# Optimization experiments

Hardware: AMD Instinct MI355X
Metric: run time of the kernel (lower is better)

## Reference

```python
import jax, jax.numpy as jnp
import numpy as np

EMB_DIM = 64
B, S, D = 64, 1024, 64

def setup_inputs() -> dict:
    key = jax.random.key(0)
    k1, k2, k3, k4, k5 = jax.random.split(key, 5)
    return {
        "query": jax.random.normal(k1, (B, S, D), dtype=jnp.float32),
        "key": jax.random.normal(k2, (B, S, D), dtype=jnp.float32),
        "value": jax.random.normal(k3, (B, S, D), dtype=jnp.float32),
        "a_key": jax.random.normal(k4, (S, S, D), dtype=jnp.float32),
        "a_value": jax.random.normal(k5, (S, S, D), dtype=jnp.float32),
    }

def reference(query, key, value, a_key, a_value):
    scale = jnp.sqrt(jnp.asarray(EMB_DIM, dtype=query.dtype))
    # standard content-content scores: [B, Sq, Sk]
    qk = jnp.einsum("bqd,bkd->bqk", query, key)
    # relative key scores: a_key is [Sq, Sk, D]; contract over D per query position
    rel_qk = jnp.einsum("bqd,qkd->bqk", query, a_key)
    attn = jax.nn.softmax((qk + rel_qk) / scale, axis=-1)
    # content values + relative values
    qkv = jnp.einsum("bqk,bkd->bqd", attn, value)
    rel_qkv = jnp.einsum("bqk,qkd->bqd", attn, a_value)
    return qkv + rel_qkv, attn
```

## Files before the change

### kernel.cpp

```cpp
#include <hip/hip_runtime.h>
#include <stdint.h>

#define S_ 1024
#define D_ 64
#define B_ 64

typedef short short8 __attribute__((ext_vector_type(8)));
typedef unsigned short ushort8 __attribute__((ext_vector_type(8)));
typedef float f32x4 __attribute__((ext_vector_type(4)));

__device__ __forceinline__ unsigned short f2bf(float x) {
    uint32_t u = __builtin_bit_cast(uint32_t, x);
    return (unsigned short)((u + 0x7FFFu + ((u >> 16) & 1u)) >> 16);
}
__device__ __forceinline__ float bf2f(unsigned short b) {
    return __builtin_bit_cast(float, ((uint32_t)b) << 16);
}
__device__ __forceinline__ uint32_t pack2(float a, float b) {
    return (uint32_t)f2bf(a) | ((uint32_t)f2bf(b) << 16);
}
__device__ __forceinline__ int scidx(int row, int k) {
    return (((row << 10) + (k & ~7)) ^ ((row & 15) << 3)) + (k & 7);
}

__global__ __launch_bounds__(256) void k1_qk(const float* __restrict__ Q,
                                             const float* __restrict__ Kk,
                                             float* __restrict__ qk) {
    __shared__ __align__(16) unsigned short Qs[128][72];
    __shared__ __align__(16) unsigned short Ks[128][72];
    const int bx = blockIdx.x;
    const int b  = bx >> 6;
    const int q0 = ((bx >> 3) & 7) << 7;
    const int k0 = (bx & 7) << 7;
    const int t  = threadIdx.x;
#pragma unroll
    for (int i = 0; i < 8; ++i) {
        int f = (i << 8) + t;
        int row = f >> 4, c = (f & 15) << 2;
        float4 v = *reinterpret_cast<const float4*>(&Q[((size_t)(b * S_ + q0 + row) << 6) + c]);
        *reinterpret_cast<uint2*>(&Qs[row][c]) = make_uint2(pack2(v.x, v.y), pack2(v.z, v.w));
        float4 u = *reinterpret_cast<const float4*>(&Kk[((size_t)(b * S_ + k0 + row) << 6) + c]);
        *reinterpret_cast<uint2*>(&Ks[row][c]) = make_uint2(pack2(u.x, u.y), pack2(u.z, u.w));
    }
    __syncthreads();
    const int l = t & 63, w = t >> 6, lr = l & 15, lg = l >> 4;
    short8 a[2][2];
#pragma unroll
    for (int mi = 0; mi < 2; ++mi)
#pragma unroll
        for (int h = 0; h < 2; ++h)
            a[mi][h] = *reinterpret_cast<const short8*>(&Qs[((w * 2 + mi) << 4) + lr][h * 32 + lg * 8]);
    f32x4 acc[2][8] = {};
#pragma unroll
    for (int n = 0; n < 8; ++n) {
        short8 b0 = *reinterpret_cast<const short8*>(&Ks[(n << 4) + lr][lg * 8]);
        short8 b1 = *reinterpret_cast<const short8*>(&Ks[(n << 4) + lr][32 + lg * 8]);
#pragma unroll
        for (int mi = 0; mi < 2; ++mi) {
            acc[mi][n] = __builtin_amdgcn_mfma_f32_16x16x32_bf16(a[mi][0], b0, acc[mi][n], 0, 0, 0);
            acc[mi][n] = __builtin_amdgcn_mfma_f32_16x16x32_bf16(a[mi][1], b1, acc[mi][n], 0, 0, 0);
        }
    }
#pragma unroll
    for (int mi = 0; mi < 2; ++mi)
#pragma unroll
        for (int n = 0; n < 8; ++n)
#pragma unroll
            for (int r = 0; r < 4; ++r) {
                int qq = q0 + ((w * 2 + mi) << 4) + (lg << 2) + r;
                int kc = k0 + (n << 4) + lr;
                qk[((size_t)(b * S_ + qq) << 10) + kc] = acc[mi][n][r];
            }
}

__device__ __forceinline__ void tpose_store(unsigned short (*Tls)[72], float4 p,
                                            int i, int t) {
    const int l = t & 63, w = t >> 6, lr = l & 15, lg = l >> 4;
    float v0 = p.x, v1 = p.y, v2 = p.z, v3 = p.w;
    float y0 = __shfl_xor(v0, 16), y1 = __shfl_xor(v1, 16),
          y2 = __shfl_xor(v2, 16), y3 = __shfl_xor(v3, 16);
    bool o = (lg & 1);
    float n0 = o ? y1 : v0, n1 = o ? v1 : y0, n2 = o ? y3 : v2, n3 = o ? v3 : y2;
    float z0 = __shfl_xor(n0, 32), z1 = __shfl_xor(n1, 32),
          z2 = __shfl_xor(n2, 32), z3 = __shfl_xor(n3, 32);
    bool h = (lg & 2);
    float T0 = h ? z2 : n0, T1 = h ? z3 : n1, T2 = h ? n2 : z0, T3 = h ? n3 : z1;
    int d = (lr << 2) + lg, kb = (i << 4) + (w << 2);
    *reinterpret_cast<uint2*>(&Tls[d][kb]) = make_uint2(pack2(T0, T1), pack2(T2, T3));
}

__global__ __launch_bounds__(256) void k2_mid(const float* __restrict__ Q,
                                              const float* __restrict__ AK,
                                              const float* __restrict__ AV,
                                              float* __restrict__ attn,
                                              float* __restrict__ outp) {
    __shared__ __align__(16) unsigned short Sc[32 * 1024];
    __shared__ __align__(16) unsigned short Qs[32][72];
    __shared__ __align__(16) unsigned short Ak[64][72];
    __shared__ float invs[32];
    const float SCL = 0.18033688011112042f;
    const int j = blockIdx.x;
    const int xcd = j & 7, slot = j >> 3;
    const int q  = xcd * 128 + (slot >> 1);
    const int b0 = (slot & 1) << 5;
    const int t  = threadIdx.x;
    const int l = t & 63, w = t >> 6, lr = l & 15, lg = l >> 4;

#pragma unroll
    for (int i = 0; i < 2; ++i) {
        int f = (i << 8) + t;
        int row = f >> 4, c = (f & 15) << 2;
        float4 v = *reinterpret_cast<const float4*>(&Q[((size_t)((b0 + row) * S_ + q) << 6) + c]);
        *reinterpret_cast<uint2*>(&Qs[row][c]) =
            make_uint2(pack2(v.x * SCL, v.y * SCL), pack2(v.z * SCL, v.w * SCL));
    }
#pragma unroll
    for (int i = 0; i < 32; ++i) {
        int col = t << 2;
        float4 v = *reinterpret_cast<const float4*>(&attn[((size_t)((b0 + i) * S_ + q) << 10) + col]);
        *reinterpret_cast<uint2*>(&Sc[scidx(i, col)]) =
            make_uint2(pack2(v.x * SCL, v.y * SCL), pack2(v.z * SCL, v.w * SCL));
    }
    const float* akbase = &AK[(size_t)q << 16];
    float4 pf[4];
#pragma unroll
    for (int i = 0; i < 4; ++i) {
        int f = (i << 8) + t;
        pf[i] = *reinterpret_cast<const float4*>(&akbase[((size_t)(f >> 4) << 6) + ((f & 15) << 2)]);
    }
    __syncthreads();

    short8 qa[2][2];
#pragma unroll
    for (int mi = 0; mi < 2; ++mi)
#pragma unroll
        for (int h = 0; h < 2; ++h)
            qa[mi][h] = *reinterpret_cast<const short8*>(&Qs[(mi << 4) + lr][(h << 5) + (lg << 3)]);

    for (int tt = 0; tt < 16; ++tt) {
        __syncthreads();
#pragma unroll
        for (int i = 0; i < 4; ++i) {
            int f = (i << 8) + t;
            int row = f >> 4, c = (f & 15) << 2;
            *reinterpret_cast<uint2*>(&Ak[row][c]) =
                make_uint2(pack2(pf[i].x, pf[i].y), pack2(pf[i].z, pf[i].w));
        }
        __syncthreads();
        if (tt < 15) {
            const float* nb = akbase + (((size_t)(tt + 1)) << 12);
#pragma unroll
            for (int i = 0; i < 4; ++i) {
                int f = (i << 8) + t;
                pf[i] = *reinterpret_cast<const float4*>(&nb[((size_t)(f >> 4) << 6) + ((f & 15) << 2)]);
            }
        }
        short8 bb0 = *reinterpret_cast<const short8*>(&Ak[(w << 4) + lr][lg << 3]);
        short8 bb1 = *reinterpret_cast<const short8*>(&Ak[(w << 4) + lr][32 + (lg << 3)]);
        int kcol = (tt << 6) + (w << 4) + lr;
#pragma unroll
        for (int mi = 0; mi < 2; ++mi) {
            f32x4 c;
#pragma unroll
            for (int r = 0; r < 4; ++r) c[r] = bf2f(Sc[scidx((mi << 4) + (lg << 2) + r, kcol)]);
            c = __builtin_amdgcn_mfma_f32_16x16x32_bf16(qa[mi][0], bb0, c, 0, 0, 0);
            c = __builtin_amdgcn_mfma_f32_16x16x32_bf16(qa[mi][1], bb1, c, 0, 0, 0);
#pragma unroll
            for (int r = 0; r < 4; ++r) Sc[scidx((mi << 4) + (lg << 2) + r, kcol)] = f2bf(c[r]);
        }
    }
    __syncthreads();

    {
        int row = t >> 3, ch = t & 7;
        float m = -1e30f;
#pragma unroll
        for (int i = 0; i < 16; ++i) {
            int k = (((i << 3) + ch) << 3);
            ushort8 v = *reinterpret_cast<const ushort8*>(&Sc[scidx(row, k)]);
#pragma unroll
            for (int jj = 0; jj < 8; ++jj) m = fmaxf(m, bf2f(v[jj]));
        }
#pragma unroll
        for (int d = 1; d < 8; d <<= 1) m = fmaxf(m, __shfl_xor(m, d));
        float s = 0.f;
#pragma unroll
        for (int i = 0; i < 16; ++i) {
            int k = (((i << 3) + ch) << 3);
            int idx = scidx(row, k);
            ushort8 v = *reinterpret_cast<const ushort8*>(&Sc[idx]);
            ushort8 e;
#pragma unroll
            for (int jj = 0; jj < 8; ++jj) {
                float ev = exp2f(bf2f(v[jj]) - m);
                s += ev;
                e[jj] = f2bf(ev);
            }
            *reinterpret_cast<ushort8*>(&Sc[idx]) = e;
        }
#pragma unroll
        for (int d = 1; d < 8; d <<= 1) s += __shfl_xor(s, d);
        float inv = 1.0f / s;
        if (ch == 0) invs[row] = inv;
    }
    __syncthreads();

    const float* avbase = &AV[(size_t)q << 16];
#pragma unroll
    for (int i = 0; i < 4; ++i) {
        int f = (i << 8) + t;
        pf[i] = *reinterpret_cast<const float4*>(&avbase[((size_t)(f >> 4) << 6) + ((f & 15) << 2)]);
    }
#pragma unroll
    for (int i = 0; i < 32; ++i) {
        int col = t << 2;
        uint2 u = *reinterpret_cast<const uint2*>(&Sc[scidx(i, col)]);
        float inv = invs[i];
        float4 o = make_float4(bf2f((unsigned short)(u.x & 0xffff)) * inv,
                               bf2f((unsigned short)(u.x >> 16)) * inv,
                               bf2f((unsigned short)(u.y & 0xffff)) * inv,
                               bf2f((unsigned short)(u.y >> 16)) * inv);
        *reinterpret_cast<float4*>(&attn[((size_t)((b0 + i) * S_ + q) << 10) + col]) = o;
    }

    f32x4 oacc[2] = {};
    for (int tt = 0; tt < 16; ++tt) {
        __syncthreads();
#pragma unroll
        for (int i = 0; i < 4; ++i) tpose_store(Ak, pf[i], i, t);
        __syncthreads();
        if (tt < 15) {
            const float* nb = avbase + (((size_t)(tt + 1)) << 12);
#pragma unroll
            for (int i = 0; i < 4; ++i) {
                int f = (i << 8) + t;
                pf[i] = *reinterpret_cast<const float4*>(&nb[((size_t)(f >> 4) << 6) + ((f & 15) << 2)]);
            }
        }
        short8 bb0 = *reinterpret_cast<const short8*>(&Ak[(w << 4) + lr][lg << 3]);
        short8 bb1 = *reinterpret_cast<const short8*>(&Ak[(w << 4) + lr][32 + (lg << 3)]);
#pragma unroll
        for (int mi = 0; mi < 2; ++mi) {
            short8 ea0 = *reinterpret_cast<const short8*>(&Sc[scidx((mi << 4) + lr, (tt << 6) + (lg << 3))]);
            short8 ea1 = *reinterpret_cast<const short8*>(&Sc[scidx((mi << 4) + lr, (tt << 6) + 32 + (lg << 3))]);
            oacc[mi] = __builtin_amdgcn_mfma_f32_16x16x32_bf16(ea0, bb0, oacc[mi], 0, 0, 0);
            oacc[mi] = __builtin_amdgcn_mfma_f32_16x16x32_bf16(ea1, bb1, oacc[mi], 0, 0, 0);
        }
    }
#pragma unroll
    for (int mi = 0; mi < 2; ++mi)
#pragma unroll
        for (int r = 0; r < 4; ++r) {
            int brow = (mi << 4) + (lg << 2) + r;
            outp[((size_t)((b0 + brow) * S_ + q) << 6) + (w << 4) + lr] = oacc[mi][r] * invs[brow];
        }
}

__global__ __launch_bounds__(256) void k3_pv(const float* __restrict__ V,
                                             const float* __restrict__ attn,
                                             float* __restrict__ outp) {
    __shared__ __align__(16) unsigned short At[64][72];
    __shared__ __align__(16) unsigned short Vt[64][72];
    const int b  = blockIdx.x >> 4;
    const int q0 = (blockIdx.x & 15) << 6;
    const int t  = threadIdx.x;
    const int l = t & 63, w = t >> 6, lr = l & 15, lg = l >> 4;
    float4 pa[4], pv[4];
#pragma unroll
    for (int i = 0; i < 4; ++i) {
        int f = (i << 8) + t;
        int row = f >> 4, c = (f & 15) << 2;
        pa[i] = *reinterpret_cast<const float4*>(&attn[((size_t)(b * S_ + q0 + row) << 10) + c]);
        pv[i] = *reinterpret_cast<const float4*>(&V[((size_t)(b * S_ + row) << 6) + c]);
    }
    f32x4 acc[4] = {};
    for (int tt = 0; tt < 16; ++tt) {
        __syncthreads();
#pragma unroll
        for (int i = 0; i < 4; ++i) {
            int f = (i << 8) + t;
            int row = f >> 4, c = (f & 15) << 2;
            *reinterpret_cast<uint2*>(&At[row][c]) =
                make_uint2(pack2(pa[i].x, pa[i].y), pack2(pa[i].z, pa[i].w));
            tpose_store(Vt, pv[i], i, t);
        }
        __syncthreads();
        if (tt < 15) {
#pragma unroll
            for (int i = 0; i < 4; ++i) {
                int f = (i << 8) + t;
                int row = f >> 4, c = (f & 15) << 2;
                pa[i] = *reinterpret_cast<const float4*>(
                    &attn[((size_t)(b * S_ + q0 + row) << 10) + ((tt + 1) << 6) + c]);
                pv[i] = *reinterpret_cast<const float4*>(
                    &V[((size_t)(b * S_ + ((tt + 1) << 6) + row) << 6) + c]);
            }
        }
        short8 a0 = *reinterpret_cast<const short8*>(&At[(w << 4) + lr][lg * 8]);
        short8 a1 = *reinterpret_cast<const short8*>(&At[(w << 4) + lr][32 + lg * 8]);
#pragma unroll
        for (int n = 0; n < 4; ++n) {
            short8 b0 = *reinterpret_cast<const short8*>(&Vt[(n << 4) + lr][lg * 8]);
            short8 b1 = *reinterpret_cast<const short8*>(&Vt[(n << 4) + lr][32 + lg * 8]);
            acc[n] = __builtin_amdgcn_mfma_f32_16x16x32_bf16(a0, b0, acc[n], 0, 0, 0);
            acc[n] = __builtin_amdgcn_mfma_f32_16x16x32_bf16(a1, b1, acc[n], 0, 0, 0);
        }
    }
#pragma unroll
    for (int n = 0; n < 4; ++n)
#pragma unroll
        for (int r = 0; r < 4; ++r) {
            size_t idx = ((size_t)(b * S_ + q0 + (w << 4) + (lg << 2) + r) << 6) + (n << 4) + lr;
            outp[idx] += acc[n][r];
        }
}

extern "C" void kernel_launch(void* const* d_in, const int* in_sizes, int n_in,
                              void* d_out, int out_size, void* d_ws, size_t ws_size,
                              hipStream_t stream) {
    (void)in_sizes; (void)n_in; (void)out_size; (void)d_ws; (void)ws_size;
    const float* Q  = (const float*)d_in[0];
    const float* K  = (const float*)d_in[1];
    const float* V  = (const float*)d_in[2];
    const float* AK = (const float*)d_in[3];
    const float* AV = (const float*)d_in[4];
    float* outp = (float*)d_out;
    float* attn = outp + (size_t)B_ * S_ * D_;

    k1_qk <<<dim3(64 * 8 * 8), dim3(256), 0, stream>>>(Q, K, attn);
    k2_mid<<<dim3(2048),       dim3(256), 0, stream>>>(Q, AK, AV, attn, outp);
    k3_pv <<<dim3(64 * 16),    dim3(256), 0, stream>>>(V, attn, outp);
}
```

Baseline: 425.7 us.

## Double-buffer relative key/value prefetch and fuse qk add into softmax pass

```diff
diff --git a/kernel.cpp b/kernel.cpp
--- a/kernel.cpp
+++ b/kernel.cpp
@@ -8,6 +8,9 @@
 typedef short short8 __attribute__((ext_vector_type(8)));
 typedef unsigned short ushort8 __attribute__((ext_vector_type(8)));
 typedef float f32x4 __attribute__((ext_vector_type(4)));
+
+#define LBAR() do { asm volatile("s_waitcnt lgkmcnt(0)" ::: "memory"); \
+                    __builtin_amdgcn_s_barrier(); } while (0)
 
 __device__ __forceinline__ unsigned short f2bf(float x) {
     uint32_t u = __builtin_bit_cast(uint32_t, x);
@@ -114,80 +117,105 @@
         *reinterpret_cast<uint2*>(&Qs[row][c]) =
             make_uint2(pack2(v.x * SCL, v.y * SCL), pack2(v.z * SCL, v.w * SCL));
     }
-#pragma unroll
-    for (int i = 0; i < 32; ++i) {
-        int col = t << 2;
-        float4 v = *reinterpret_cast<const float4*>(&attn[((size_t)((b0 + i) * S_ + q) << 10) + col]);
-        *reinterpret_cast<uint2*>(&Sc[scidx(i, col)]) =
-            make_uint2(pack2(v.x * SCL, v.y * SCL), pack2(v.z * SCL, v.w * SCL));
-    }
     const float* akbase = &AK[(size_t)q << 16];
-    float4 pf[4];
-#pragma unroll
-    for (int i = 0; i < 4; ++i) {
-        int f = (i << 8) + t;
-        pf[i] = *reinterpret_cast<const float4*>(&akbase[((size_t)(f >> 4) << 6) + ((f & 15) << 2)]);
-    }
-    __syncthreads();
-
+    float4 pf[2][4];
+#pragma unroll
+    for (int d2 = 0; d2 < 2; ++d2)
+#pragma unroll
+        for (int i = 0; i < 4; ++i) {
+            int f = (i << 8) + t;
+            pf[d2][i] = *reinterpret_cast<const float4*>(
+                &akbase[(size_t)(d2 << 12) + ((size_t)(f >> 4) << 6) + ((f & 15) << 2)]);
+        }
+    LBAR();
     short8 qa[2][2];
 #pragma unroll
-    for (int mi = 0; mi < 2; ++mi)
+    for (int bh = 0; bh < 2; ++bh)
 #pragma unroll
         for (int h = 0; h < 2; ++h)
-            qa[mi][h] = *reinterpret_cast<const short8*>(&Qs[(mi << 4) + lr][(h << 5) + (lg << 3)]);
+            qa[bh][h] = *reinterpret_cast<const short8*>(&Qs[(bh << 4) + lr][(h << 5) + (lg << 3)]);
 
     for (int tt = 0; tt < 16; ++tt) {
-        __syncthreads();
+        LBAR();
 #pragma unroll
         for (int i = 0; i < 4; ++i) {
             int f = (i << 8) + t;
             int row = f >> 4, c = (f & 15) << 2;
             *reinterpret_cast<uint2*>(&Ak[row][c]) =
-                make_uint2(pack2(pf[i].x, pf[i].y), pack2(pf[i].z, pf[i].w));
-        }
-        __syncthreads();
-        if (tt < 15) {
-            const float* nb = akbase + (((size_t)(tt + 1)) << 12);
+                make_uint2(pack2(pf[tt & 1][i].x, pf[tt & 1][i].y),
+                           pack2(pf[tt & 1][i].z, pf[tt & 1][i].w));
+        }
+        LBAR();
+        if (tt < 14) {
+            const float* nb = akbase + (((size_t)(tt + 2)) << 12);
 #pragma unroll
             for (int i = 0; i < 4; ++i) {
                 int f = (i << 8) + t;
-                pf[i] = *reinterpret_cast<const float4*>(&nb[((size_t)(f >> 4) << 6) + ((f & 15) << 2)]);
-            }
-        }
-        short8 bb0 = *reinterpret_cast<const short8*>(&Ak[(w << 4) + lr][lg << 3]);
-        short8 bb1 = *reinterpret_cast<const short8*>(&Ak[(w << 4) + lr][32 + (lg << 3)]);
-        int kcol = (tt << 6) + (w << 4) + lr;
-#pragma unroll
-        for (int mi = 0; mi < 2; ++mi) {
-            f32x4 c;
-#pragma unroll
-            for (int r = 0; r < 4; ++r) c[r] = bf2f(Sc[scidx((mi << 4) + (lg << 2) + r, kcol)]);
-            c = __builtin_amdgcn_mfma_f32_16x16x32_bf16(qa[mi][0], bb0, c, 0, 0, 0);
-            c = __builtin_amdgcn_mfma_f32_16x16x32_bf16(qa[mi][1], bb1, c, 0, 0, 0);
-#pragma unroll
-            for (int r = 0; r < 4; ++r) Sc[scidx((mi << 4) + (lg << 2) + r, kcol)] = f2bf(c[r]);
-        }
-    }
-    __syncthreads();
+                pf[tt & 1][i] = *reinterpret_cast<const float4*>(
+                    &nb[((size_t)(f >> 4) << 6) + ((f & 15) << 2)]);
+            }
+        }
+        short8 ak0 = *reinterpret_cast<const short8*>(&Ak[(w << 4) + lr][lg << 3]);
+        short8 ak1 = *reinterpret_cast<const short8*>(&Ak[(w << 4) + lr][32 + (lg << 3)]);
+        int kbase = (tt << 6) + (w << 4) + (lg << 2);
+#pragma unroll
+        for (int bh = 0; bh < 2; ++bh) {
+            f32x4 c = {};
+            c = __builtin_amdgcn_mfma_f32_16x16x32_bf16(ak0, qa[bh][0], c, 0, 0, 0);
+            c = __builtin_amdgcn_mfma_f32_16x16x32_bf16(ak1, qa[bh][1], c, 0, 0, 0);
+            *reinterpret_cast<uint2*>(&Sc[scidx((bh << 4) + lr, kbase)]) =
+                make_uint2(pack2(c[0], c[1]), pack2(c[2], c[3]));
+        }
+    }
+    LBAR();
+
+    const float* avbase = &AV[(size_t)q << 16];
+    float4 pv[2][4];
+#pragma unroll
+    for (int d2 = 0; d2 < 2; ++d2)
+#pragma unroll
+        for (int i = 0; i < 4; ++i) {
+            int f = (i << 8) + t;
+            pv[d2][i] = *reinterpret_cast<const float4*>(
+                &avbase[(size_t)(d2 << 12) + ((size_t)(f >> 4) << 6) + ((f & 15) << 2)]);
+        }
 
     {
         int row = t >> 3, ch = t & 7;
+        float* qkrow = &attn[((size_t)((b0 + row) * S_ + q) << 10)];
         float m = -1e30f;
-#pragma unroll
+        float4 g0 = *reinterpret_cast<const float4*>(&qkrow[ch << 3]);
+        float4 g1 = *reinterpret_cast<const float4*>(&qkrow[(ch << 3) + 4]);
         for (int i = 0; i < 16; ++i) {
-            int k = (((i << 3) + ch) << 3);
-            ushort8 v = *reinterpret_cast<const ushort8*>(&Sc[scidx(row, k)]);
-#pragma unroll
-            for (int jj = 0; jj < 8; ++jj) m = fmaxf(m, bf2f(v[jj]));
+            float4 c0 = g0, c1 = g1;
+            if (i < 15) {
+                int kn = (((i + 1) << 3) + ch) << 3;
+                g0 = *reinterpret_cast<const float4*>(&qkrow[kn]);
+                g1 = *reinterpret_cast<const float4*>(&qkrow[kn + 4]);
+            }
+            int idx = scidx(row, ((i << 3) + ch) << 3);
+            ushort8 rel = *reinterpret_cast<const ushort8*>(&Sc[idx]);
+            float s0 = fmaf(c0.x, SCL, bf2f(rel[0]));
+            float s1 = fmaf(c0.y, SCL, bf2f(rel[1]));
+            float s2 = fmaf(c0.z, SCL, bf2f(rel[2]));
+            float s3 = fmaf(c0.w, SCL, bf2f(rel[3]));
+            float s4 = fmaf(c1.x, SCL, bf2f(rel[4]));
+            float s5 = fmaf(c1.y, SCL, bf2f(rel[5]));
+            float s6 = fmaf(c1.z, SCL, bf2f(rel[6]));
+            float s7 = fmaf(c1.w, SCL, bf2f(rel[7]));
+            m = fmaxf(m, fmaxf(fmaxf(fmaxf(s0, s1), fmaxf(s2, s3)),
+                               fmaxf(fmaxf(s4, s5), fmaxf(s6, s7))));
+            ushort8 o;
+            o[0] = f2bf(s0); o[1] = f2bf(s1); o[2] = f2bf(s2); o[3] = f2bf(s3);
+            o[4] = f2bf(s4); o[5] = f2bf(s5); o[6] = f2bf(s6); o[7] = f2bf(s7);
+            *reinterpret_cast<ushort8*>(&Sc[idx]) = o;
         }
 #pragma unroll
         for (int d = 1; d < 8; d <<= 1) m = fmaxf(m, __shfl_xor(m, d));
         float s = 0.f;
-#pragma unroll
+#pragma unroll 4
         for (int i = 0; i < 16; ++i) {
-            int k = (((i << 3) + ch) << 3);
-            int idx = scidx(row, k);
+            int idx = scidx(row, ((i << 3) + ch) << 3);
             ushort8 v = *reinterpret_cast<const ushort8*>(&Sc[idx]);
             ushort8 e;
 #pragma unroll
@@ -202,39 +230,32 @@
         for (int d = 1; d < 8; d <<= 1) s += __shfl_xor(s, d);
         float inv = 1.0f / s;
         if (ch == 0) invs[row] = inv;
-    }
-    __syncthreads();
-
-    const float* avbase = &AV[(size_t)q << 16];
-#pragma unroll
-    for (int i = 0; i < 4; ++i) {
-        int f = (i << 8) + t;
-        pf[i] = *reinterpret_cast<const float4*>(&avbase[((size_t)(f >> 4) << 6) + ((f & 15) << 2)]);
-    }
-#pragma unroll
-    for (int i = 0; i < 32; ++i) {
-        int col = t << 2;
-        uint2 u = *reinterpret_cast<const uint2*>(&Sc[scidx(i, col)]);
-        float inv = invs[i];
-        float4 o = make_float4(bf2f((unsigned short)(u.x & 0xffff)) * inv,
-                               bf2f((unsigned short)(u.x >> 16)) * inv,
-                               bf2f((unsigned short)(u.y & 0xffff)) * inv,
-                               bf2f((unsigned short)(u.y >> 16)) * inv);
-        *reinterpret_cast<float4*>(&attn[((size_t)((b0 + i) * S_ + q) << 10) + col]) = o;
+#pragma unroll 4
+        for (int i = 0; i < 16; ++i) {
+            int k = ((i << 3) + ch) << 3;
+            ushort8 v = *reinterpret_cast<const ushort8*>(&Sc[scidx(row, k)]);
+            float4 o0 = make_float4(bf2f(v[0]) * inv, bf2f(v[1]) * inv,
+                                    bf2f(v[2]) * inv, bf2f(v[3]) * inv);
+            float4 o1 = make_float4(bf2f(v[4]) * inv, bf2f(v[5]) * inv,
+                                    bf2f(v[6]) * inv, bf2f(v[7]) * inv);
+            *reinterpret_cast<float4*>(&qkrow[k]) = o0;
+            *reinterpret_cast<float4*>(&qkrow[k + 4]) = o1;
+        }
     }
 
     f32x4 oacc[2] = {};
     for (int tt = 0; tt < 16; ++tt) {
-        __syncthreads();
-#pragma unroll
-        for (int i = 0; i < 4; ++i) tpose_store(Ak, pf[i], i, t);
-        __syncthreads();
-        if (tt < 15) {
-            const float* nb = avbase + (((size_t)(tt + 1)) << 12);
+        LBAR();
+#pragma unroll
+        for (int i = 0; i < 4; ++i) tpose_store(Ak, pv[tt & 1][i], i, t);
+        LBAR();
+        if (tt < 14) {
+            const float* nb = avbase + (((size_t)(tt + 2)) << 12);
 #pragma unroll
             for (int i = 0; i < 4; ++i) {
                 int f = (i << 8) + t;
-                pf[i] = *reinterpret_cast<const float4*>(&nb[((size_t)(f >> 4) << 6) + ((f & 15) << 2)]);
+                pv[tt & 1][i] = *reinterpret_cast<const float4*>(
+                    &nb[((size_t)(f >> 4) << 6) + ((f & 15) << 2)]);
             }
         }
         short8 bb0 = *reinterpret_cast<const short8*>(&Ak[(w << 4) + lr][lg << 3]);
@@ -275,7 +296,7 @@
     }
     f32x4 acc[4] = {};
     for (int tt = 0; tt < 16; ++tt) {
-        __syncthreads();
+        LBAR();
 #pragma unroll
         for (int i = 0; i < 4; ++i) {
             int f = (i << 8) + t;
@@ -284,7 +305,7 @@
                 make_uint2(pack2(pa[i].x, pa[i].y), pack2(pa[i].z, pa[i].w));
             tpose_store(Vt, pv[i], i, t);
         }
-        __syncthreads();
+        LBAR();
         if (tt < 15) {
 #pragma unroll
             for (int i = 0; i < 4; ++i) {
```

Measured after the change: 648.9 us. +52.4%, slower.

## Fuse content scores into exp pass and drop max-subtraction in softmax

Applied to the files above, without the earlier changes.

```diff
diff --git a/kernel.cpp b/kernel.cpp
--- a/kernel.cpp
+++ b/kernel.cpp
@@ -114,13 +114,6 @@
         *reinterpret_cast<uint2*>(&Qs[row][c]) =
             make_uint2(pack2(v.x * SCL, v.y * SCL), pack2(v.z * SCL, v.w * SCL));
     }
-#pragma unroll
-    for (int i = 0; i < 32; ++i) {
-        int col = t << 2;
-        float4 v = *reinterpret_cast<const float4*>(&attn[((size_t)((b0 + i) * S_ + q) << 10) + col]);
-        *reinterpret_cast<uint2*>(&Sc[scidx(i, col)]) =
-            make_uint2(pack2(v.x * SCL, v.y * SCL), pack2(v.z * SCL, v.w * SCL));
-    }
     const float* akbase = &AK[(size_t)q << 16];
     float4 pf[4];
 #pragma unroll
@@ -129,13 +122,12 @@
         pf[i] = *reinterpret_cast<const float4*>(&akbase[((size_t)(f >> 4) << 6) + ((f & 15) << 2)]);
     }
     __syncthreads();
-
     short8 qa[2][2];
 #pragma unroll
-    for (int mi = 0; mi < 2; ++mi)
+    for (int bh = 0; bh < 2; ++bh)
 #pragma unroll
         for (int h = 0; h < 2; ++h)
-            qa[mi][h] = *reinterpret_cast<const short8*>(&Qs[(mi << 4) + lr][(h << 5) + (lg << 3)]);
+            qa[bh][h] = *reinterpret_cast<const short8*>(&Qs[(bh << 4) + lr][(h << 5) + (lg << 3)]);
 
     for (int tt = 0; tt < 16; ++tt) {
         __syncthreads();
@@ -155,63 +147,59 @@
                 pf[i] = *reinterpret_cast<const float4*>(&nb[((size_t)(f >> 4) << 6) + ((f & 15) << 2)]);
             }
         }
-        short8 bb0 = *reinterpret_cast<const short8*>(&Ak[(w << 4) + lr][lg << 3]);
-        short8 bb1 = *reinterpret_cast<const short8*>(&Ak[(w << 4) + lr][32 + (lg << 3)]);
-        int kcol = (tt << 6) + (w << 4) + lr;
-#pragma unroll
-        for (int mi = 0; mi < 2; ++mi) {
-            f32x4 c;
-#pragma unroll
-            for (int r = 0; r < 4; ++r) c[r] = bf2f(Sc[scidx((mi << 4) + (lg << 2) + r, kcol)]);
-            c = __builtin_amdgcn_mfma_f32_16x16x32_bf16(qa[mi][0], bb0, c, 0, 0, 0);
-            c = __builtin_amdgcn_mfma_f32_16x16x32_bf16(qa[mi][1], bb1, c, 0, 0, 0);
-#pragma unroll
-            for (int r = 0; r < 4; ++r) Sc[scidx((mi << 4) + (lg << 2) + r, kcol)] = f2bf(c[r]);
-        }
+        short8 ak0 = *reinterpret_cast<const short8*>(&Ak[(w << 4) + lr][lg << 3]);
+        short8 ak1 = *reinterpret_cast<const short8*>(&Ak[(w << 4) + lr][32 + (lg << 3)]);
+        int kbase = (tt << 6) + (w << 4) + (lg << 2);
+#pragma unroll
+        for (int bh = 0; bh < 2; ++bh) {
+            f32x4 c = {};
+            c = __builtin_amdgcn_mfma_f32_16x16x32_bf16(ak0, qa[bh][0], c, 0, 0, 0);
+            c = __builtin_amdgcn_mfma_f32_16x16x32_bf16(ak1, qa[bh][1], c, 0, 0, 0);
+            *reinterpret_cast<uint2*>(&Sc[scidx((bh << 4) + lr, kbase)]) =
+                make_uint2(pack2(c[0], c[1]), pack2(c[2], c[3]));
+        }
+    }
+    __syncthreads();
+
+    const float* avbase = &AV[(size_t)q << 16];
+    float4 pv[4];
+#pragma unroll
+    for (int i = 0; i < 4; ++i) {
+        int f = (i << 8) + t;
+        pv[i] = *reinterpret_cast<const float4*>(
+            &avbase[((size_t)(f >> 4) << 6) + ((f & 15) << 2)]);
+    }
+
+#pragma unroll 8
+    for (int i = 0; i < 32; ++i) {
+        int col = t << 2;
+        float4 g = *reinterpret_cast<const float4*>(&attn[((size_t)((b0 + i) * S_ + q) << 10) + col]);
+        int idx = scidx(i, col);
+        uint2 cu = *reinterpret_cast<const uint2*>(&Sc[idx]);
+        float p0 = exp2f(fmaf(g.x, SCL, bf2f((unsigned short)(cu.x & 0xffff))));
+        float p1 = exp2f(fmaf(g.y, SCL, bf2f((unsigned short)(cu.x >> 16))));
+        float p2 = exp2f(fmaf(g.z, SCL, bf2f((unsigned short)(cu.y & 0xffff))));
+        float p3 = exp2f(fmaf(g.w, SCL, bf2f((unsigned short)(cu.y >> 16))));
+        *reinterpret_cast<uint2*>(&Sc[idx]) = make_uint2(pack2(p0, p1), pack2(p2, p3));
     }
     __syncthreads();
 
     {
         int row = t >> 3, ch = t & 7;
-        float m = -1e30f;
-#pragma unroll
+        float s = 0.f;
+#pragma unroll 4
         for (int i = 0; i < 16; ++i) {
-            int k = (((i << 3) + ch) << 3);
-            ushort8 v = *reinterpret_cast<const ushort8*>(&Sc[scidx(row, k)]);
-#pragma unroll
-            for (int jj = 0; jj < 8; ++jj) m = fmaxf(m, bf2f(v[jj]));
-        }
-#pragma unroll
-        for (int d = 1; d < 8; d <<= 1) m = fmaxf(m, __shfl_xor(m, d));
-        float s = 0.f;
-#pragma unroll
-        for (int i = 0; i < 16; ++i) {
-            int k = (((i << 3) + ch) << 3);
-            int idx = scidx(row, k);
-            ushort8 v = *reinterpret_cast<const ushort8*>(&Sc[idx]);
-            ushort8 e;
-#pragma unroll
-            for (int jj = 0; jj < 8; ++jj) {
-                float ev = exp2f(bf2f(v[jj]) - m);
-                s += ev;
-                e[jj] = f2bf(ev);
-            }
-            *reinterpret_cast<ushort8*>(&Sc[idx]) = e;
+            ushort8 v = *reinterpret_cast<const ushort8*>(&Sc[scidx(row, (((i << 3) + ch) << 3))]);
+#pragma unroll
+            for (int jj = 0; jj < 8; ++jj) s += bf2f(v[jj]);
         }
 #pragma unroll
         for (int d = 1; d < 8; d <<= 1) s += __shfl_xor(s, d);
-        float inv = 1.0f / s;
-        if (ch == 0) invs[row] = inv;
-    }
-    __syncthreads();
-
-    const float* avbase = &AV[(size_t)q << 16];
-#pragma unroll
-    for (int i = 0; i < 4; ++i) {
-        int f = (i << 8) + t;
-        pf[i] = *reinterpret_cast<const float4*>(&avbase[((size_t)(f >> 4) << 6) + ((f & 15) << 2)]);
-    }
-#pragma unroll
+        if (ch == 0) invs[row] = 1.0f / s;
+    }
+    __syncthreads();
+
+#pragma unroll 8
     for (int i = 0; i < 32; ++i) {
         int col = t << 2;
         uint2 u = *reinterpret_cast<const uint2*>(&Sc[scidx(i, col)]);
@@ -227,14 +215,15 @@
     for (int tt = 0; tt < 16; ++tt) {
         __syncthreads();
 #pragma unroll
-        for (int i = 0; i < 4; ++i) tpose_store(Ak, pf[i], i, t);
+        for (int i = 0; i < 4; ++i) tpose_store(Ak, pv[i], i, t);
         __syncthreads();
         if (tt < 15) {
             const float* nb = avbase + (((size_t)(tt + 1)) << 12);
 #pragma unroll
             for (int i = 0; i < 4; ++i) {
                 int f = (i << 8) + t;
-                pf[i] = *reinterpret_cast<const float4*>(&nb[((size_t)(f >> 4) << 6) + ((f & 15) << 2)]);
+                pv[i] = *reinterpret_cast<const float4*>(
+                    &nb[((size_t)(f >> 4) << 6) + ((f & 15) << 2)]);
             }
         }
         short8 bb0 = *reinterpret_cast<const short8*>(&Ak[(w << 4) + lr][lg << 3]);
```

Measured after the change: 453.5 us. 6.5% more time.
